# Kernel tuning notes

Measured on AMD Instinct MI355X. Metric: run time of the kernel, lower is better.

Reference implementation:

```python
import jax, jax.numpy as jnp
import numpy as np

B, T, E, H = 256, 128, 300, 512


def setup_inputs() -> dict:
    key = jax.random.key(0)
    ks = jax.random.split(key, 7)
    x = jax.random.normal(ks[0], (B, T, E), jnp.float32)
    stdv_p = 1.0 / np.sqrt(E)      # torch Linear default: U(-1/sqrt(fan_in), ...)
    stdv_r = 1.0 / np.sqrt(H)      # TreeLSTMCell.reset_parameters: U(-1/sqrt(H), ...)
    W_proj = jax.random.uniform(ks[1], (E, H), jnp.float32, -stdv_p, stdv_p)
    b_proj = jax.random.uniform(ks[2], (H,), jnp.float32, -stdv_p, stdv_p)
    W_gate = jax.random.uniform(ks[3], (E, H), jnp.float32, -stdv_p, stdv_p)
    b_gate = jax.random.uniform(ks[4], (H,), jnp.float32, -stdv_p, stdv_p)
    W_reduce = jax.random.uniform(ks[5], (2 * H, 5 * H), jnp.float32, -stdv_r, stdv_r)
    b_reduce = jax.random.uniform(ks[6], (5 * H,), jnp.float32, -stdv_r, stdv_r)
    # Valid shift-reduce sequence for a left-branching binary tree over T tokens:
    # shift, shift, (reduce, shift)*(T-2), reduce  -> T shifts, T-1 reduces, len 2T-1
    seq = np.array([0, 0] + [1, 0] * (T - 2) + [1], dtype=np.int32)
    transitions = jnp.asarray(np.tile(seq[:, None], (1, B)))  # [2T-1, B]
    return {"x": x, "W_proj": W_proj, "b_proj": b_proj, "W_gate": W_gate,
            "b_gate": b_gate, "W_reduce": W_reduce, "b_reduce": b_reduce,
            "transitions": transitions}


def reference(x, W_proj, b_proj, W_gate, b_gate, W_reduce, b_reduce, transitions):
    Bx, Tx, _ = x.shape
    Hh = W_proj.shape[1]
    # leaf states: c = proj_x(x); h = sigmoid(proj_x_gate(x)) * tanh(c)
    c_buf = x @ W_proj + b_proj                                   # [B,T,H]
    h_buf = jax.nn.sigmoid(x @ W_gate + b_gate) * jnp.tanh(c_buf)  # [B,T,H]
    buffers = jnp.concatenate([h_buf, c_buf], axis=-1)            # [B,T,2H]
    bidx = jnp.arange(Bx)

    def cell(left, right):
        # TreeLSTMCell: reduce_layer(cat(h_l, h_r)) -> i, f_l, f_r, g, o
        h_l, c_l = left[:, :Hh], left[:, Hh:]
        h_r, c_r = right[:, :Hh], right[:, Hh:]
        proj = jnp.concatenate([h_l, h_r], axis=-1) @ W_reduce + b_reduce  # [B,5H]
        i, f_l, f_r, g, o = jnp.split(proj, 5, axis=-1)
        c = (jax.nn.sigmoid(f_l) * c_l + jax.nn.sigmoid(f_r) * c_r
             + jax.nn.sigmoid(i) * jnp.tanh(g))
        h = jax.nn.sigmoid(o) * jnp.tanh(c)
        return jnp.concatenate([h, c], axis=-1)

    def step(carry, trans_t):
        stack, sp, bp = carry
        # shift: buffer.pop() takes the LAST remaining token
        shifted = buffers[bidx, bp - 1]                      # [B,2H]
        left = stack[bidx, jnp.maximum(sp - 2, 0)]
        right = stack[bidx, jnp.maximum(sp - 1, 0)]
        reduced = cell(left, right)
        is_shift = trans_t == 0                              # [B] bool
        new_val = jnp.where(is_shift[:, None], shifted, reduced)
        pos = jnp.where(is_shift, sp, jnp.maximum(sp - 2, 0))
        stack = stack.at[bidx, pos].set(new_val)
        sp = jnp.where(is_shift, sp + 1, sp - 1)
        bp = jnp.where(is_shift, bp - 1, bp)
        return (stack, sp, bp), None

    stack0 = jnp.zeros((Bx, Tx, 2 * Hh), x.dtype)
    sp0 = jnp.zeros((Bx,), jnp.int32)
    bp0 = jnp.full((Bx,), Tx, jnp.int32)
    (stack, sp, bp), _ = jax.lax.scan(step, (stack0, sp0, bp0), transitions)
    # final root: h half of top-of-stack
    return stack[bidx, sp - 1][:, :Hh]
```

## Files before the change

kernel.cpp:

```cpp
#include <hip/hip_runtime.h>

typedef unsigned short ushort_t;
typedef unsigned long long u64_t;
typedef __attribute__((ext_vector_type(8))) short short8;
typedef __attribute__((ext_vector_type(4))) float floatx4;

#define B_ 256
#define T_ 128
#define E_ 300
#define H_ 512
#define NE_ 127
#define NT_ 255
#define SLH_ 260
#define SLC_ 130
#define ZCODE_ 1023
#define PREVF_ 0x10000

__device__ inline ushort_t f2bf(float f){
  unsigned u = __builtin_bit_cast(unsigned, f);
  unsigned r = u + 0x7FFFu + ((u >> 16) & 1u);
  return (ushort_t)(r >> 16);
}
__device__ inline float bf2f(ushort_t h){
  unsigned u = ((unsigned)h) << 16;
  return __builtin_bit_cast(float, u);
}
__device__ inline float sigm(float x){ return 1.0f / (1.0f + __expf(-x)); }
__device__ inline float ftanh(float x){
  float e = __expf(2.0f * x);
  return 1.0f - 2.0f / (e + 1.0f);
}

__device__ inline void store_h_coh64(u64_t* p, u64_t v){
  __hip_atomic_store(p, v, __ATOMIC_RELAXED, __HIP_MEMORY_SCOPE_AGENT);
}

__global__ __launch_bounds__(256) void xcast_kernel(const float* __restrict__ x,
    ushort_t* __restrict__ xb){
  int t = blockIdx.x * 256 + threadIdx.x;
  if (t >= (B_ * T_) * 40) return;
  int row = t / 40, k8 = (t % 40) * 8;
  const float* src = x + (size_t)row * E_;
  short8 v;
  #pragma unroll
  for (int j = 0; j < 8; ++j){
    int k = k8 + j;
    v[j] = (k < E_) ? (short)f2bf(src[k]) : (short)0;
  }
  *(short8*)(xb + (size_t)row * 320 + k8) = v;
}

__global__ __launch_bounds__(256) void pack_w_kernel(const float* __restrict__ W,
    ushort_t* __restrict__ dst, int K, int N, int NS, int total){
  int t = blockIdx.x * 256 + threadIdx.x;
  if (t >= total) return;
  int L = t & 63;
  int s = (t >> 6) % NS;
  int ct = t / (64 * NS);
  int n = ct * 16 + (L & 15);
  int kbase = s * 32 + ((L >> 4) << 3);
  short8 pack;
  #pragma unroll
  for (int j = 0; j < 8; ++j){
    int k = kbase + j;
    pack[j] = (k < K) ? (short)f2bf(W[(size_t)k * N + n]) : (short)0;
  }
  *(short8*)(dst + (size_t)t * 8) = pack;
}

__global__ void sched_kernel(const int* __restrict__ trans, int* __restrict__ lsel,
    int* __restrict__ rsel, int* __restrict__ wph, int* __restrict__ rootsel){
  __shared__ int stk[32 * 128];
  __shared__ int stkid[32 * 128];
  int tid = threadIdx.x;
  int b0 = blockIdx.x * 32;
  int b = b0 + tid;
  for (int i = 0; i < 128; ++i){ stk[tid * 128 + i] = ZCODE_; stkid[tid * 128 + i] = -1; }
  u64_t tog0 = 0, tog1 = 0;
  int sp = 0, bp = T_, e = 0;
  for (int t = 0; t < NT_; ++t){
    int tr = trans[t * B_ + b];
    if (tr == 0){
      int pos = sp; if (pos < 0) pos = 0; if (pos > 127) pos = 127;
      stk[tid * 128 + pos] = bp - 1;
      stkid[tid * 128 + pos] = bp - 1;
      sp += 1; bp -= 1;
    } else {
      int i2 = sp - 2; if (i2 < 0) i2 = 0; if (i2 > 127) i2 = 127;
      int i1 = sp - 1; if (i1 < 0) i1 = 0; if (i1 > 127) i1 = 127;
      if (e < NE_){
        int lc = stk[tid * 128 + i2], rc = stk[tid * 128 + i1];
        int lid = stkid[tid * 128 + i2], rid = stkid[tid * 128 + i1];
        int previd = T_ + e - 1;
        lsel[e * B_ + b] = lc | ((e > 0 && lid == previd) ? PREVF_ : 0);
        rsel[e * B_ + b] = rc | ((e > 0 && rid == previd) ? PREVF_ : 0);
        int pos = i2;
        unsigned ob;
        if (pos < 64){ ob = (unsigned)((tog0 >> pos) & 1); tog0 ^= (1ull << pos); }
        else         { ob = (unsigned)((tog1 >> (pos - 64)) & 1); tog1 ^= (1ull << (pos - 64)); }
        int phys = pos * 2 + (int)(ob ^ 1u);
        wph[e * B_ + b] = phys;
        stk[tid * 128 + pos] = 256 + phys;
        stkid[tid * 128 + pos] = T_ + e;
      }
      e += 1; sp -= 1;
    }
  }
  for (int k = e; k < NE_; ++k){
    lsel[k * B_ + b] = ZCODE_; rsel[k * B_ + b] = ZCODE_;
    wph[k * B_ + b] = 256;
  }
  int ip = sp - 1; if (ip < 0) ip = 0; if (ip > 127) ip = 127;
  rootsel[b] = stk[tid * 128 + ip];
}

__global__ __launch_bounds__(256) void leaf_kernel(const ushort_t* __restrict__ xb,
    const ushort_t* __restrict__ WpP, const ushort_t* __restrict__ WgP,
    const float* __restrict__ b_proj, const float* __restrict__ b_gate,
    ushort_t* __restrict__ leaf_h, ushort_t* __restrict__ leaf_c){
  int wave = threadIdx.x >> 6, lane = threadIdx.x & 63;
  int r0 = blockIdx.x * 64 + wave * 16;
  int cbase = blockIdx.y * 8;
  int arow = r0 + (lane & 15);
  int klane = (lane >> 4) << 3;
  const ushort_t* xrow = xb + (size_t)arow * 320;
  floatx4 accP[8], accG[8];
  #pragma unroll
  for (int i = 0; i < 8; ++i){ accP[i] = (floatx4){0,0,0,0}; accG[i] = (floatx4){0,0,0,0}; }
  #pragma unroll
  for (int s = 0; s < 10; ++s){
    short8 a = *(const short8*)(xrow + s * 32 + klane);
    #pragma unroll
    for (int cc = 0; cc < 8; ++cc){
      short8 bp = *(const short8*)(WpP + (((size_t)(cbase + cc) * 10 + s) * 64 + lane) * 8);
      accP[cc] = __builtin_amdgcn_mfma_f32_16x16x32_bf16(a, bp, accP[cc], 0, 0, 0);
      short8 bg = *(const short8*)(WgP + (((size_t)(cbase + cc) * 10 + s) * 64 + lane) * 8);
      accG[cc] = __builtin_amdgcn_mfma_f32_16x16x32_bf16(a, bg, accG[cc], 0, 0, 0);
    }
  }
  int rbase = r0 + ((lane >> 4) << 2);
  #pragma unroll
  for (int cc = 0; cc < 8; ++cc){
    int col = (cbase + cc) * 16 + (lane & 15);
    float bp = b_proj[col], bg = b_gate[col];
    #pragma unroll
    for (int r = 0; r < 4; ++r){
      int row = rbase + r;
      float cv = accP[cc][r] + bp;
      float hv = sigm(accG[cc][r] + bg) * ftanh(cv);
      size_t o = (size_t)row * H_ + col;
      leaf_c[o] = f2bf(cv);
      leaf_h[o] = f2bf(hv);
    }
  }
}

__global__ __launch_bounds__(256, 1) void chain_kernel(
    const ushort_t* __restrict__ WrP, const float* __restrict__ b_reduce,
    const ushort_t* __restrict__ leaf_h, const ushort_t* __restrict__ leaf_c,
    ushort_t* __restrict__ slot_h, float* __restrict__ slot_c,
    const int* __restrict__ lsel, const int* __restrict__ rsel,
    const int* __restrict__ wph, const ushort_t* __restrict__ zbuf,
    unsigned* __restrict__ gflags){
  __shared__ floatx4 part[4][2][5][64];
  __shared__ ushort_t hp[4][8][16] __attribute__((aligned(8)));
  const int bid  = blockIdx.x;
  const int cth  = bid >> 3;
  const int rg   = bid & 7;
  const int kq   = threadIdx.x >> 6;
  const int lane = threadIdx.x & 63;
  const int m16  = lane & 15;
  const int klane = (lane >> 4) << 3;
  const int colh = cth * 16 + m16;
  const int row0 = rg * 32;
  const int* ssel = (kq < 2) ? rsel : lsel;
  const int qK    = (kq < 2) ? (2 + kq) : (kq - 2);
  const int kcolbase = (kq & 1) * 256;
  float bias[5];
  #pragma unroll
  for (int g = 0; g < 5; ++g) bias[g] = b_reduce[g * H_ + colh];
  unsigned* myflag  = gflags + ((unsigned)(rg * 32 + cth) << 5);
  unsigned* pollptr = gflags + ((unsigned)(rg * 32 + (kq & 1) * 16 + m16) << 5);
  const int err_ = lane >> 4;
  float creg[2] = {0.0f, 0.0f};

  #pragma unroll 1
  for (int e = 0; e < NE_; ++e){
    int code[2];
    const ushort_t* leafp[2];
    #pragma unroll
    for (int rt = 0; rt < 2; ++rt){
      int row = row0 + rt * 16 + m16;
      code[rt] = ssel[e * B_ + row] & 0x3FF;
      leafp[rt] = (code[rt] < 128) ? leaf_h + ((size_t)row * T_ + code[rt]) * H_ + kcolbase
                                   : zbuf;
    }
    const bool isnode0 = (code[0] >= 256 && code[0] < 512);
    const bool isnode1 = (code[1] >= 256 && code[1] < 512);

    short8 Wreg[5][8];
    #pragma unroll
    for (int g = 0; g < 5; ++g)
      #pragma unroll
      for (int s = 0; s < 8; ++s)
        Wreg[g][s] = *(const short8*)(WrP + (((size_t)(g * 32 + cth) * 32 + qK * 8 + s) * 64 + lane) * 8);
    #pragma unroll
    for (int g = 0; g < 5; ++g)
      asm volatile("" : "+v"(Wreg[g][0]), "+v"(Wreg[g][1]), "+v"(Wreg[g][2]),
                        "+v"(Wreg[g][3]), "+v"(Wreg[g][4]), "+v"(Wreg[g][5]),
                        "+v"(Wreg[g][6]), "+v"(Wreg[g][7]));

    union AB { u64_t q[16]; short8 v[8]; };
    AB ab[2];
    #pragma unroll
    for (int rt = 0; rt < 2; ++rt){
      if (!(rt == 0 ? isnode0 : isnode1)){
        #pragma unroll
        for (int s = 0; s < 8; ++s) ab[rt].v[s] = *(const short8*)(leafp[rt] + s * 32 + klane);
      }
    }

    float cl[2], cr[2];
    int wv[2];
    #pragma unroll
    for (int rix = 0; rix < 2; ++rix){
      const int R  = kq * 8 + err_ * 2 + rix;
      const int bb = row0 + R;
      const int ls = lsel[e * B_ + bb], rs = rsel[e * B_ + bb];
      wv[rix] = wph[e * B_ + bb];
      int lc = ls & 0x3FF, rc = rs & 0x3FF;
      float lv = 0.0f, rv = 0.0f;
      if (ls & PREVF_) lv = creg[rix];
      else if (lc < 128) lv = bf2f(leaf_c[((size_t)bb * T_ + lc) * H_ + colh]);
      else if (lc < 512) lv = slot_c[((size_t)bb * SLC_ + ((lc - 256) >> 1)) * H_ + colh];
      if (rs & PREVF_) rv = creg[rix];
      else if (rc < 128) rv = bf2f(leaf_c[((size_t)bb * T_ + rc) * H_ + colh]);
      else if (rc < 512) rv = slot_c[((size_t)bb * SLC_ + ((rc - 256) >> 1)) * H_ + colh];
      cl[rix] = lv; cr[rix] = rv;
    }

    floatx4 acc[2][5];
    #pragma unroll
    for (int rt = 0; rt < 2; ++rt)
      #pragma unroll
      for (int g = 0; g < 5; ++g) acc[rt][g] = (floatx4){0,0,0,0};
    #pragma unroll
    for (int rt = 0; rt < 2; ++rt){
      if (!(rt == 0 ? isnode0 : isnode1)){
        #pragma unroll
        for (int s = 0; s < 8; ++s)
          #pragma unroll
          for (int g = 0; g < 5; ++g)
            acc[rt][g] = __builtin_amdgcn_mfma_f32_16x16x32_bf16(ab[rt].v[s], Wreg[g][s], acc[rt][g], 0, 0, 0);
        #pragma unroll
        for (int g = 0; g < 5; ++g) part[kq][rt][g][lane] = acc[rt][g];
      }
    }

    if (isnode0 || isnode1){
      const unsigned tgt = (unsigned)e;
      int it = 0;
      for (;;){
        unsigned v = __hip_atomic_load(pollptr, __ATOMIC_RELAXED, __HIP_MEMORY_SCOPE_AGENT);
        if (__all(v >= tgt)) break;
        if (it < 2)       __builtin_amdgcn_s_sleep(0);
        else if (it < 16) __builtin_amdgcn_s_sleep(2);
        else              __builtin_amdgcn_s_sleep(8);
        ++it;
      }
    }

    #pragma unroll
    for (int rt = 0; rt < 2; ++rt){
      if (rt == 0 ? isnode0 : isnode1){
        int row = row0 + rt * 16 + m16;
        const ushort_t* p = slot_h + ((size_t)row * SLH_ + (code[rt] - 256)) * H_ + kcolbase + klane;
        #pragma unroll
        for (int s = 0; s < 8; ++s){
          ab[rt].q[2 * s]     = __hip_atomic_load((const u64_t*)(p + s * 32),
                                  __ATOMIC_RELAXED, __HIP_MEMORY_SCOPE_AGENT);
          ab[rt].q[2 * s + 1] = __hip_atomic_load((const u64_t*)(p + s * 32 + 4),
                                  __ATOMIC_RELAXED, __HIP_MEMORY_SCOPE_AGENT);
        }
        #pragma unroll
        for (int s = 0; s < 8; ++s)
          #pragma unroll
          for (int g = 0; g < 5; ++g)
            acc[rt][g] = __builtin_amdgcn_mfma_f32_16x16x32_bf16(ab[rt].v[s], Wreg[g][s], acc[rt][g], 0, 0, 0);
        #pragma unroll
        for (int g = 0; g < 5; ++g) part[kq][rt][g][lane] = acc[rt][g];
      }
    }
    __syncthreads();

    #pragma unroll
    for (int rix = 0; rix < 2; ++rix){
      const int R    = kq * 8 + err_ * 2 + rix;
      const int bb   = row0 + R;
      const int rt2  = R >> 4;
      const int lane2 = (((R >> 2) & 3) << 4) + m16;
      const int rsub = R & 3;
      float o[5];
      #pragma unroll
      for (int g = 0; g < 5; ++g)
        o[g] = part[0][rt2][g][lane2][rsub] + part[1][rt2][g][lane2][rsub]
             + part[2][rt2][g][lane2][rsub] + part[3][rt2][g][lane2][rsub] + bias[g];
      float cn = sigm(o[1]) * cl[rix] + sigm(o[2]) * cr[rix] + sigm(o[0]) * ftanh(o[3]);
      float hn = sigm(o[4]) * ftanh(cn);
      creg[rix] = cn;
      slot_c[((size_t)bb * SLC_ + (wv[rix] >> 1)) * H_ + colh] = cn;
      hp[kq][err_ * 2 + rix][m16] = f2bf(hn);
    }
    if (lane < 32){
      int rl = lane >> 2, qw = lane & 3;
      int bb2 = row0 + kq * 8 + rl;
      int w2 = wph[e * B_ + bb2];
      ushort_t* dst = slot_h + ((size_t)bb2 * SLH_ + w2) * H_ + cth * 16 + qw * 4;
      u64_t qv = *(const u64_t*)&hp[kq][rl][qw * 4];
      store_h_coh64((u64_t*)dst, qv);
    }
    asm volatile("s_waitcnt vmcnt(0)" ::: "memory");
    __syncthreads();
    if (threadIdx.x == 0)
      __hip_atomic_store(myflag, (unsigned)(e + 1),
                         __ATOMIC_RELAXED, __HIP_MEMORY_SCOPE_AGENT);
  }
}

__global__ __launch_bounds__(256) void final_kernel(const int* __restrict__ rootsel,
    const ushort_t* __restrict__ leaf_h, const ushort_t* __restrict__ slot_h,
    float* __restrict__ out){
  int i = blockIdx.x * 256 + threadIdx.x;
  if (i >= B_ * H_) return;
  int b = i >> 9, j = i & (H_ - 1);
  int code = rootsel[b] & 0x3FF;
  float v = 0.0f;
  if (code < 128)      v = bf2f(leaf_h[((size_t)b * T_ + code) * H_ + j]);
  else if (code < 512) v = bf2f(slot_h[((size_t)b * SLH_ + (code - 256)) * H_ + j]);
  out[i] = v;
}

extern "C" void kernel_launch(void* const* d_in, const int* in_sizes, int n_in,
                              void* d_out, int out_size, void* d_ws, size_t ws_size,
                              hipStream_t stream){
  const float* x        = (const float*)d_in[0];
  const float* W_proj   = (const float*)d_in[1];
  const float* b_proj   = (const float*)d_in[2];
  const float* W_gate   = (const float*)d_in[3];
  const float* b_gate   = (const float*)d_in[4];
  const float* W_reduce = (const float*)d_in[5];
  const float* b_reduce = (const float*)d_in[6];
  const int*   trans    = (const int*)d_in[7];
  float* out = (float*)d_out;

  char* ws = (char*)d_ws;
  size_t o = 0;
  ushort_t* WpP    = (ushort_t*)(ws + o); o += (size_t)32*10*64*8*2;
  ushort_t* WgP    = (ushort_t*)(ws + o); o += (size_t)32*10*64*8*2;
  ushort_t* WrP    = (ushort_t*)(ws + o); o += (size_t)160*32*64*8*2;
  ushort_t* leaf_h = (ushort_t*)(ws + o); o += (size_t)B_*T_*H_*2;
  ushort_t* leaf_c = (ushort_t*)(ws + o); o += (size_t)B_*T_*H_*2;
  ushort_t* slot_h = (ushort_t*)(ws + o); o += (size_t)B_*SLH_*H_*2;
  float*    slot_c = (float*)(ws + o);    o += (size_t)B_*SLC_*H_*4;
  int* lsel    = (int*)(ws + o); o += (size_t)NE_*B_*4;
  int* rsel    = (int*)(ws + o); o += (size_t)NE_*B_*4;
  int* wph     = (int*)(ws + o); o += (size_t)NE_*B_*4;
  int* rootsel = (int*)(ws + o); o += (size_t)B_*4;
  unsigned* gflags = (unsigned*)(ws + o); o += (size_t)8 * 32 * 128;
  ushort_t* zbuf = (ushort_t*)(ws + o); o += 2048;
  ushort_t* xb = (ushort_t*)slot_c;
  (void)ws_size; (void)in_sizes; (void)n_in; (void)out_size;

  hipMemsetAsync(gflags, 0, (size_t)8 * 32 * 128, stream);
  hipMemsetAsync(zbuf, 0, 2048, stream);
  xcast_kernel<<<((B_*T_)*40 + 255)/256, 256, 0, stream>>>(x, xb);
  pack_w_kernel<<<(32*10*64 + 255)/256, 256, 0, stream>>>(W_proj, WpP, 300, 512, 10, 32*10*64);
  pack_w_kernel<<<(32*10*64 + 255)/256, 256, 0, stream>>>(W_gate, WgP, 300, 512, 10, 32*10*64);
  pack_w_kernel<<<(160*32*64 + 255)/256, 256, 0, stream>>>(W_reduce, WrP, 1024, 2560, 32, 160*32*64);
  sched_kernel<<<8, 32, 0, stream>>>(trans, lsel, rsel, wph, rootsel);
  leaf_kernel<<<dim3(512, 4), 256, 0, stream>>>(xb, WpP, WgP, b_proj, b_gate, leaf_h, leaf_c);
  chain_kernel<<<256, 256, 0, stream>>>(WrP, b_reduce, leaf_h, leaf_c, slot_h, slot_c,
                                        lsel, rsel, wph, zbuf, gflags);
  final_kernel<<<(B_*H_ + 255)/256, 256, 0, stream>>>(rootsel, leaf_h, slot_h, out);
}
```

Before: 1.172 ms.

## Hoist weight registers out of loop, prefetch next leaf operands, transpose LDS partials

The bf16 reduce-weight fragments are now loaded into registers once before the step loop instead of on every step. Leaf h operands for step e+1 are fetched during step e into a second register set, so the load latency overlaps with the current MFMA, spin-wait and cell work. The LDS partial-sum array is stored as [r][lane] scalars rather than floatx4, which changes the access pattern when the four K-quarter partials are reduced. Keeping two sets of A operands raises VGPR pressure in a block already holding 40 short8 weight registers, which could cause spills.

```diff
diff --git a/kernel.cpp b/kernel.cpp
--- a/kernel.cpp
+++ b/kernel.cpp
@@ -162,7 +162,7 @@
     const int* __restrict__ lsel, const int* __restrict__ rsel,
     const int* __restrict__ wph, const ushort_t* __restrict__ zbuf,
     unsigned* __restrict__ gflags){
-  __shared__ floatx4 part[4][2][5][64];
+  __shared__ float parts[4][2][5][4][64];
   __shared__ ushort_t hp[4][8][16] __attribute__((aligned(8)));
   const int bid  = blockIdx.x;
   const int cth  = bid >> 3;
@@ -184,41 +184,38 @@
   const int err_ = lane >> 4;
   float creg[2] = {0.0f, 0.0f};
 
+  short8 Wreg[5][8];
+  #pragma unroll
+  for (int g = 0; g < 5; ++g)
+    #pragma unroll
+    for (int s = 0; s < 8; ++s)
+      Wreg[g][s] = *(const short8*)(WrP + (((size_t)(g * 32 + cth) * 32 + qK * 8 + s) * 64 + lane) * 8);
+  #pragma unroll
+  for (int g = 0; g < 5; ++g)
+    asm volatile("" : "+v"(Wreg[g][0]), "+v"(Wreg[g][1]), "+v"(Wreg[g][2]),
+                      "+v"(Wreg[g][3]), "+v"(Wreg[g][4]), "+v"(Wreg[g][5]),
+                      "+v"(Wreg[g][6]), "+v"(Wreg[g][7]));
+
+  union AB { u64_t q[16]; short8 v[8]; };
+  AB abc[2], abn[2];
+  int code[2];
+
+  #pragma unroll
+  for (int rt = 0; rt < 2; ++rt){
+    int row = row0 + rt * 16 + m16;
+    code[rt] = ssel[0 * B_ + row] & 0x3FF;
+    const ushort_t* lp = (code[rt] < 128) ? leaf_h + ((size_t)row * T_ + code[rt]) * H_ + kcolbase
+                                          : zbuf;
+    if (code[rt] < 256 || code[rt] >= 512){
+      #pragma unroll
+      for (int s = 0; s < 8; ++s) abc[rt].v[s] = *(const short8*)(lp + s * 32 + klane);
+    }
+  }
+
   #pragma unroll 1
   for (int e = 0; e < NE_; ++e){
-    int code[2];
-    const ushort_t* leafp[2];
-    #pragma unroll
-    for (int rt = 0; rt < 2; ++rt){
-      int row = row0 + rt * 16 + m16;
-      code[rt] = ssel[e * B_ + row] & 0x3FF;
-      leafp[rt] = (code[rt] < 128) ? leaf_h + ((size_t)row * T_ + code[rt]) * H_ + kcolbase
-                                   : zbuf;
-    }
     const bool isnode0 = (code[0] >= 256 && code[0] < 512);
     const bool isnode1 = (code[1] >= 256 && code[1] < 512);
-
-    short8 Wreg[5][8];
-    #pragma unroll
-    for (int g = 0; g < 5; ++g)
-      #pragma unroll
-      for (int s = 0; s < 8; ++s)
-        Wreg[g][s] = *(const short8*)(WrP + (((size_t)(g * 32 + cth) * 32 + qK * 8 + s) * 64 + lane) * 8);
-    #pragma unroll
-    for (int g = 0; g < 5; ++g)
-      asm volatile("" : "+v"(Wreg[g][0]), "+v"(Wreg[g][1]), "+v"(Wreg[g][2]),
-                        "+v"(Wreg[g][3]), "+v"(Wreg[g][4]), "+v"(Wreg[g][5]),
-                        "+v"(Wreg[g][6]), "+v"(Wreg[g][7]));
-
-    union AB { u64_t q[16]; short8 v[8]; };
-    AB ab[2];
-    #pragma unroll
-    for (int rt = 0; rt < 2; ++rt){
-      if (!(rt == 0 ? isnode0 : isnode1)){
-        #pragma unroll
-        for (int s = 0; s < 8; ++s) ab[rt].v[s] = *(const short8*)(leafp[rt] + s * 32 + klane);
-      }
-    }
 
     float cl[2], cr[2];
     int wv[2];
@@ -239,6 +236,21 @@
       cl[rix] = lv; cr[rix] = rv;
     }
 
+    int ncode[2] = {code[0], code[1]};
+    if (e + 1 < NE_){
+      #pragma unroll
+      for (int rt = 0; rt < 2; ++rt){
+        int row = row0 + rt * 16 + m16;
+        ncode[rt] = ssel[(e + 1) * B_ + row] & 0x3FF;
+        const ushort_t* lp = (ncode[rt] < 128) ? leaf_h + ((size_t)row * T_ + ncode[rt]) * H_ + kcolbase
+                                               : zbuf;
+        if (ncode[rt] < 256 || ncode[rt] >= 512){
+          #pragma unroll
+          for (int s = 0; s < 8; ++s) abn[rt].v[s] = *(const short8*)(lp + s * 32 + klane);
+        }
+      }
+    }
+
     floatx4 acc[2][5];
     #pragma unroll
     for (int rt = 0; rt < 2; ++rt)
@@ -251,9 +263,12 @@
         for (int s = 0; s < 8; ++s)
           #pragma unroll
           for (int g = 0; g < 5; ++g)
-            acc[rt][g] = __builtin_amdgcn_mfma_f32_16x16x32_bf16(ab[rt].v[s], Wreg[g][s], acc[rt][g], 0, 0, 0);
+            acc[rt][g] = __builtin_amdgcn_mfma_f32_16x16x32_bf16(abc[rt].v[s], Wreg[g][s], acc[rt][g], 0, 0, 0);
         #pragma unroll
-        for (int g = 0; g < 5; ++g) part[kq][rt][g][lane] = acc[rt][g];
+        for (int g = 0; g < 5; ++g)
+          #pragma unroll
+          for (int r = 0; r < 4; ++r)
+            parts[kq][rt][g][r][lane] = acc[rt][g][r];
       }
     }
 
@@ -277,18 +292,21 @@
         const ushort_t* p = slot_h + ((size_t)row * SLH_ + (code[rt] - 256)) * H_ + kcolbase + klane;
         #pragma unroll
         for (int s = 0; s < 8; ++s){
-          ab[rt].q[2 * s]     = __hip_atomic_load((const u64_t*)(p + s * 32),
+          abc[rt].q[2 * s]     = __hip_atomic_load((const u64_t*)(p + s * 32),
                                   __ATOMIC_RELAXED, __HIP_MEMORY_SCOPE_AGENT);
-          ab[rt].q[2 * s + 1] = __hip_atomic_load((const u64_t*)(p + s * 32 + 4),
+          abc[rt].q[2 * s + 1] = __hip_atomic_load((const u64_t*)(p + s * 32 + 4),
                                   __ATOMIC_RELAXED, __HIP_MEMORY_SCOPE_AGENT);
         }
         #pragma unroll
         for (int s = 0; s < 8; ++s)
           #pragma unroll
           for (int g = 0; g < 5; ++g)
-            acc[rt][g] = __builtin_amdgcn_mfma_f32_16x16x32_bf16(ab[rt].v[s], Wreg[g][s], acc[rt][g], 0, 0, 0);
+            acc[rt][g] = __builtin_amdgcn_mfma_f32_16x16x32_bf16(abc[rt].v[s], Wreg[g][s], acc[rt][g], 0, 0, 0);
         #pragma unroll
-        for (int g = 0; g < 5; ++g) part[kq][rt][g][lane] = acc[rt][g];
+        for (int g = 0; g < 5; ++g)
+          #pragma unroll
+          for (int r = 0; r < 4; ++r)
+            parts[kq][rt][g][r][lane] = acc[rt][g][r];
       }
     }
     __syncthreads();
@@ -303,8 +321,8 @@
       float o[5];
       #pragma unroll
       for (int g = 0; g < 5; ++g)
-        o[g] = part[0][rt2][g][lane2][rsub] + part[1][rt2][g][lane2][rsub]
-             + part[2][rt2][g][lane2][rsub] + part[3][rt2][g][lane2][rsub] + bias[g];
+        o[g] = parts[0][rt2][g][rsub][lane2] + parts[1][rt2][g][rsub][lane2]
+             + parts[2][rt2][g][rsub][lane2] + parts[3][rt2][g][rsub][lane2] + bias[g];
       float cn = sigm(o[1]) * cl[rix] + sigm(o[2]) * cr[rix] + sigm(o[0]) * ftanh(o[3]);
       float hn = sigm(o[4]) * ftanh(cn);
       creg[rix] = cn;
@@ -324,6 +342,12 @@
     if (threadIdx.x == 0)
       __hip_atomic_store(myflag, (unsigned)(e + 1),
                          __ATOMIC_RELAXED, __HIP_MEMORY_SCOPE_AGENT);
+
+    #pragma unroll
+    for (int rt = 0; rt < 2; ++rt){
+      if (ncode[rt] < 256 || ncode[rt] >= 512) abc[rt] = abn[rt];
+      code[rt] = ncode[rt];
+    }
   }
 }
 
```

Result: no change. 1.168 ms (-0.4%).
